# Kernel tuning notes

Hardware: AMD Instinct MI355X
Metric: run time of the kernel (lower is better)

The kernel has to match this reference:

```python
import jax, jax.numpy as jnp
import numpy as np
import math

D_MODEL = 256  # projected q/k dim
D_K_IN = 32    # raw key feature dim
D_V = 64       # value projection dim
KEEP_PROB = 0.8  # dropout p=0.2

def setup_inputs() -> dict:
    key = jax.random.key(0)
    ks = jax.random.split(key, 9)
    B, Lq, Lk = 4, 4096, 4096
    s = 0.02
    return {
        "q": jax.random.normal(ks[0], (B, Lq, D_MODEL), jnp.float32),
        "k": jax.random.normal(ks[1], (B, Lk, D_K_IN), jnp.float32),
        "v": jax.random.normal(ks[2], (B, Lk, D_MODEL), jnp.float32),
        "Wq": jax.random.normal(ks[3], (D_MODEL, D_MODEL), jnp.float32) * s,
        "bq": jnp.zeros((D_MODEL,), jnp.float32),
        "Wk": jax.random.normal(ks[4], (D_K_IN, D_MODEL), jnp.float32) * s,
        "bk": jnp.zeros((D_MODEL,), jnp.float32),
        "Wv": jax.random.normal(ks[5], (D_MODEL, D_V), jnp.float32) * s,
        "bv": jnp.zeros((D_V,), jnp.float32),
    }

def reference(q, k, v, Wq, bq, Wk, bk, Wv, bv):
    # Linear projections
    qp = q @ Wq + bq                       # [B, Lq, 256]
    kp = k @ Wk + bk                       # [B, Lk, 256]
    vp = v @ Wv + bv                       # [B, Lk, 64]
    scale = 1.0 / math.sqrt(qp.shape[-1])
    scores = jnp.einsum("bqd,bkd->bqk", qp, kp) * scale  # [B, Lq, Lk]
    attn = jax.nn.softmax(scores, axis=-1)
    # dropout p=0.2 (training mode), deterministic key
    mask = jax.random.bernoulli(jax.random.key(42), KEEP_PROB, attn.shape)
    attn = jnp.where(mask, attn / KEEP_PROB, 0.0)
    return jnp.einsum("bqk,bkd->bqd", attn, vp)  # [B, Lq, 64]
```

## Files before the change

### kernel.cpp

```cpp
#include <hip/hip_runtime.h>


typedef short s16x8 __attribute__((ext_vector_type(8)));
typedef float f32x4 __attribute__((ext_vector_type(4)));

#define L    4096
#define DM   256
#define DV   64
#define MTOT 16384

__device__ __forceinline__ short f2bf(float f) {
  unsigned u = __builtin_bit_cast(unsigned, f);
  u += 0x7FFFu + ((u >> 16) & 1u);
  return (short)(u >> 16);
}

__device__ __forceinline__ unsigned rotl32c(unsigned x, int r) {
  return (x << r) | (x >> (32 - r));
}

__device__ __forceinline__ unsigned tf_keep(unsigned ctr) {
  unsigned x0 = 0u;
  unsigned x1 = ctr + 42u;
#define TFR(r) { x0 += x1; x1 = rotl32c(x1, r); x1 ^= x0; }
  TFR(13) TFR(15) TFR(26) TFR(6)
  x0 += 42u;          x1 += 0x1BD11BF1u;
  TFR(17) TFR(29) TFR(16) TFR(24)
  x0 += 0x1BD11BF0u;  x1 += 2u;
  TFR(13) TFR(15) TFR(26) TFR(6)
         x1 += 45u;
  TFR(17) TFR(29) TFR(16) TFR(24)
  x0 += 42u;          x1 += 0x1BD11BF4u;
  TFR(13) TFR(15) TFR(26) TFR(6)
  x0 += 0x1BD11BF0u;  x1 += 5u;
#undef TFR
  return ((x0 ^ x1) < 3435974144u) ? 1u : 0u;
}

template <int K, int N, bool TRANS_OUT>
__global__ __launch_bounds__(256) void proj_kernel(
    const float* __restrict__ A, const float* __restrict__ W,
    const float* __restrict__ bias, short* __restrict__ out) {
  const int lane = threadIdx.x & 63;
  const int wv   = threadIdx.x >> 6;
  const int l15 = lane & 15, l4 = lane >> 4;
  const int rowbase = blockIdx.x * 64 + wv * 16;
  constexpr int NT = N / 16;
  constexpr int KC = K / 32;
  f32x4 acc[NT];
#pragma unroll
  for (int i = 0; i < NT; ++i) acc[i] = (f32x4){0.f, 0.f, 0.f, 0.f};
  const int arow = rowbase + l15;
  for (int kc = 0; kc < KC; ++kc) {
    const f32x4* ap = (const f32x4*)(A + (size_t)arow * K + kc * 32 + l4 * 8);
    f32x4 a0 = ap[0], a1 = ap[1];
    s16x8 af;
#pragma unroll
    for (int j = 0; j < 4; ++j) { af[j] = f2bf(a0[j]); af[4 + j] = f2bf(a1[j]); }
#pragma unroll
    for (int nt = 0; nt < NT; ++nt) {
      const float* wp = W + (size_t)(kc * 32 + l4 * 8) * N + nt * 16 + l15;
      s16x8 bf;
#pragma unroll
      for (int j = 0; j < 8; ++j) bf[j] = f2bf(wp[(size_t)j * N]);
      acc[nt] = __builtin_amdgcn_mfma_f32_16x16x32_bf16(af, bf, acc[nt], 0, 0, 0);
    }
  }
#pragma unroll
  for (int nt = 0; nt < NT; ++nt) {
    const int gcol = nt * 16 + l15;
    const float bv = bias[gcol];
#pragma unroll
    for (int j = 0; j < 4; ++j) {
      const int grow = rowbase + l4 * 4 + j;
      const float vv = acc[nt][j] + bv;
      if (TRANS_OUT) {
        const int b = grow >> 12, key = grow & 4095;
        out[(size_t)(b * 64 + gcol) * L + key] = f2bf(vv);
      } else {
        out[(size_t)grow * N + gcol] = f2bf(vv);
      }
    }
  }
}

__global__ __launch_bounds__(256) void attn_kernel(
    const short* __restrict__ qp, const short* __restrict__ kp,
    const short* __restrict__ vpT, float* __restrict__ out) {
  __shared__ __align__(16) short kbuf[64 * 256];
  __shared__ __align__(16) short vbuf[64 * 64];
  __shared__ __align__(16) short pbuf[4][16 * 64];
  const int tid = threadIdx.x;
  const int lane = tid & 63, wv = tid >> 6;
  const int l15 = lane & 15, l4 = lane >> 4;
  const int qt = blockIdx.x, b = blockIdx.y;
  const int qrow0 = b * L + qt * 64 + wv * 16;

  s16x8 qf[8];
#pragma unroll
  for (int kc = 0; kc < 8; ++kc)
    qf[kc] = *(const s16x8*)(qp + (size_t)(qrow0 + l15) * DM + kc * 32 + l4 * 8);

  f32x4 accO[4];
#pragma unroll
  for (int i = 0; i < 4; ++i) accO[i] = (f32x4){0.f, 0.f, 0.f, 0.f};
  float zpart[4] = {0.f, 0.f, 0.f, 0.f};

  const unsigned qglob = (unsigned)qrow0;
  constexpr float CEXP = 0.09016844005556021f;

  for (int kb = 0; kb < 64; ++kb) {
    __syncthreads();
    {
      const short* src = kp + (size_t)(b * L + kb * 64) * DM;
#pragma unroll
      for (int it = 0; it < 8; ++it) {
        const int c = it * 256 + tid;
        const int row = c >> 5, off = (c & 31) * 8;
        const int e = (row * 256 + off) ^ ((row & 7) << 3);
        *(s16x8*)(kbuf + e) = *(const s16x8*)(src + (size_t)row * DM + off);
      }
      const short* vsrc = vpT + (size_t)b * 64 * L + kb * 64;
#pragma unroll
      for (int it = 0; it < 2; ++it) {
        const int c = it * 256 + tid;
        const int row = c >> 3, off = (c & 7) * 8;
        const int e = (row * 64 + off) ^ ((row & 7) << 3);
        *(s16x8*)(vbuf + e) = *(const s16x8*)(vsrc + (size_t)row * L + off);
      }
    }
    __syncthreads();

    f32x4 sf[4];
#pragma unroll
    for (int kt = 0; kt < 4; ++kt) sf[kt] = (f32x4){0.f, 0.f, 0.f, 0.f};
#pragma unroll
    for (int kc = 0; kc < 8; ++kc) {
#pragma unroll
      for (int kt = 0; kt < 4; ++kt) {
        const int row = kt * 16 + l15;
        const int e = (row * 256 + kc * 32 + l4 * 8) ^ ((row & 7) << 3);
        const s16x8 kf = *(const s16x8*)(kbuf + e);
        sf[kt] = __builtin_amdgcn_mfma_f32_16x16x32_bf16(qf[kc], kf, sf[kt], 0, 0, 0);
      }
    }

    unsigned keep = 0;
#pragma unroll
    for (int kt = 0; kt < 4; ++kt) {
#pragma unroll
      for (int j = 0; j < 4; ++j) {
        const unsigned q = qglob + (unsigned)(l4 * 4 + j);
        const unsigned idx = (q << 12) + (unsigned)(kb * 64 + kt * 16 + l15);
        keep |= tf_keep(idx) << (kt * 4 + j);
      }
    }

#pragma unroll
    for (int kt = 0; kt < 4; ++kt) {
#pragma unroll
      for (int j = 0; j < 4; ++j) {
        const float e = exp2f(sf[kt][j] * CEXP);
        zpart[j] += e;
        const float pd = ((keep >> (kt * 4 + j)) & 1u) ? e : 0.0f;
        const int row = l4 * 4 + j, col = kt * 16 + l15;
        const int pe = (row * 64 + col) ^ ((row & 7) << 3);
        pbuf[wv][pe] = f2bf(pd);
      }
    }
    __syncthreads();

#pragma unroll
    for (int ks = 0; ks < 2; ++ks) {
      const int pe = (l15 * 64 + ks * 32 + l4 * 8) ^ ((l15 & 7) << 3);
      const s16x8 pa = *(const s16x8*)(&pbuf[wv][0] + pe);
#pragma unroll
      for (int nt = 0; nt < 4; ++nt) {
        const int vrow = nt * 16 + l15;
        const int ve = (vrow * 64 + ks * 32 + l4 * 8) ^ ((vrow & 7) << 3);
        const s16x8 vb = *(const s16x8*)(vbuf + ve);
        accO[nt] = __builtin_amdgcn_mfma_f32_16x16x32_bf16(pa, vb, accO[nt], 0, 0, 0);
      }
    }
  }

#pragma unroll
  for (int j = 0; j < 4; ++j) {
    float z = zpart[j];
    z += __shfl_xor(z, 1);
    z += __shfl_xor(z, 2);
    z += __shfl_xor(z, 4);
    z += __shfl_xor(z, 8);
    const float inv = 1.0f / (0.8f * z);
    const int grow = qrow0 + l4 * 4 + j;
#pragma unroll
    for (int nt = 0; nt < 4; ++nt)
      out[(size_t)grow * DV + nt * 16 + l15] = accO[nt][j] * inv;
  }
}

extern "C" void kernel_launch(void* const* d_in, const int* in_sizes, int n_in,
                              void* d_out, int out_size, void* d_ws, size_t ws_size,
                              hipStream_t stream) {
  const float* q  = (const float*)d_in[0];
  const float* k  = (const float*)d_in[1];
  const float* v  = (const float*)d_in[2];
  const float* Wq = (const float*)d_in[3];
  const float* bq = (const float*)d_in[4];
  const float* Wk = (const float*)d_in[5];
  const float* bk = (const float*)d_in[6];
  const float* Wv = (const float*)d_in[7];
  const float* bv = (const float*)d_in[8];
  float* out = (float*)d_out;

  short* qp  = (short*)d_ws;
  short* kpb = qp + (size_t)MTOT * DM;
  short* vpT = kpb + (size_t)MTOT * DM;

  proj_kernel<256, 256, false><<<MTOT / 64, 256, 0, stream>>>(q, Wq, bq, qp);
  proj_kernel<32, 256, false><<<MTOT / 64, 256, 0, stream>>>(k, Wk, bk, kpb);
  proj_kernel<256, 64, true><<<MTOT / 64, 256, 0, stream>>>(v, Wv, bv, vpT);
  attn_kernel<<<dim3(64, 4), 256, 0, stream>>>(qp, kpb, vpT, out);
}
```

Measured before the change: 384.8 us.

## Split attention over key dimension and pre-transpose bf16 projection weights

The attention kernel is split four ways along the key axis (grid z). Each split writes unnormalized partial outputs and partial softmax denominators, and a new combine kernel sums them and normalizes. This lifts the grid from 256 blocks to 1024 so the GPU is better filled, and the key tile shrinks to 32 rows to cut LDS use and raise occupancy. A prep kernel converts the weights to transposed bf16 once per call, so the projection kernels can do vector loads instead of strided scalar loads with per-element conversion. The cost is extra partial-result traffic to and from global memory plus two more kernel launches.

```diff
diff --git a/kernel.cpp b/kernel.cpp
--- a/kernel.cpp
+++ b/kernel.cpp
@@ -8,6 +8,8 @@
 #define DM   256
 #define DV   64
 #define MTOT 16384
+#define KSPLIT 4
+#define KBLK 32
 
 __device__ __forceinline__ short f2bf(float f) {
   unsigned u = __builtin_bit_cast(unsigned, f);
@@ -37,9 +39,28 @@
   return ((x0 ^ x1) < 3435974144u) ? 1u : 0u;
 }
 
+__global__ __launch_bounds__(256) void prep_kernel(
+    const float* __restrict__ Wq, const float* __restrict__ Wk,
+    const float* __restrict__ Wv, short* __restrict__ wqT,
+    short* __restrict__ wkT, short* __restrict__ wvT) {
+  const int idx = blockIdx.x * 256 + threadIdx.x;
+  if (idx < 65536) {
+    const int n = idx >> 8, k = idx & 255;
+    wqT[idx] = f2bf(Wq[k * 256 + n]);
+  }
+  if (idx < 8192) {
+    const int n = idx >> 5, k = idx & 31;
+    wkT[idx] = f2bf(Wk[k * 256 + n]);
+  }
+  if (idx < 16384) {
+    const int n = idx >> 8, k = idx & 255;
+    wvT[idx] = f2bf(Wv[k * 64 + n]);
+  }
+}
+
 template <int K, int N, bool TRANS_OUT>
 __global__ __launch_bounds__(256) void proj_kernel(
-    const float* __restrict__ A, const float* __restrict__ W,
+    const float* __restrict__ A, const short* __restrict__ WT,
     const float* __restrict__ bias, short* __restrict__ out) {
   const int lane = threadIdx.x & 63;
   const int wv   = threadIdx.x >> 6;
@@ -51,6 +72,7 @@
 #pragma unroll
   for (int i = 0; i < NT; ++i) acc[i] = (f32x4){0.f, 0.f, 0.f, 0.f};
   const int arow = rowbase + l15;
+#pragma unroll
   for (int kc = 0; kc < KC; ++kc) {
     const f32x4* ap = (const f32x4*)(A + (size_t)arow * K + kc * 32 + l4 * 8);
     f32x4 a0 = ap[0], a1 = ap[1];
@@ -59,10 +81,7 @@
     for (int j = 0; j < 4; ++j) { af[j] = f2bf(a0[j]); af[4 + j] = f2bf(a1[j]); }
 #pragma unroll
     for (int nt = 0; nt < NT; ++nt) {
-      const float* wp = W + (size_t)(kc * 32 + l4 * 8) * N + nt * 16 + l15;
-      s16x8 bf;
-#pragma unroll
-      for (int j = 0; j < 8; ++j) bf[j] = f2bf(wp[(size_t)j * N]);
+      const s16x8 bf = *(const s16x8*)(WT + (size_t)(nt * 16 + l15) * K + kc * 32 + l4 * 8);
       acc[nt] = __builtin_amdgcn_mfma_f32_16x16x32_bf16(af, bf, acc[nt], 0, 0, 0);
     }
   }
@@ -84,16 +103,17 @@
   }
 }
 
-__global__ __launch_bounds__(256) void attn_kernel(
+__global__ __launch_bounds__(256, 4) void attn_kernel(
     const short* __restrict__ qp, const short* __restrict__ kp,
-    const short* __restrict__ vpT, float* __restrict__ out) {
-  __shared__ __align__(16) short kbuf[64 * 256];
-  __shared__ __align__(16) short vbuf[64 * 64];
-  __shared__ __align__(16) short pbuf[4][16 * 64];
+    const short* __restrict__ vpT, float* __restrict__ partO,
+    float* __restrict__ partZ) {
+  __shared__ __align__(16) short kbuf[KBLK * 256];
+  __shared__ __align__(16) short vbuf[64 * KBLK];
+  __shared__ __align__(16) short pbuf[4][16 * KBLK];
   const int tid = threadIdx.x;
   const int lane = tid & 63, wv = tid >> 6;
   const int l15 = lane & 15, l4 = lane >> 4;
-  const int qt = blockIdx.x, b = blockIdx.y;
+  const int qt = blockIdx.x, b = blockIdx.y, z = blockIdx.z;
   const int qrow0 = b * L + qt * 64 + wv * 16;
 
   s16x8 qf[8];
@@ -108,36 +128,34 @@
 
   const unsigned qglob = (unsigned)qrow0;
   constexpr float CEXP = 0.09016844005556021f;
-
-  for (int kb = 0; kb < 64; ++kb) {
+  const int kb0 = z * (L / KSPLIT / KBLK);
+
+  for (int i = 0; i < L / KSPLIT / KBLK; ++i) {
+    const int kbase = (kb0 + i) * KBLK;
     __syncthreads();
     {
-      const short* src = kp + (size_t)(b * L + kb * 64) * DM;
-#pragma unroll
-      for (int it = 0; it < 8; ++it) {
+      const short* src = kp + (size_t)(b * L + kbase) * DM;
+#pragma unroll
+      for (int it = 0; it < 4; ++it) {
         const int c = it * 256 + tid;
         const int row = c >> 5, off = (c & 31) * 8;
         const int e = (row * 256 + off) ^ ((row & 7) << 3);
         *(s16x8*)(kbuf + e) = *(const s16x8*)(src + (size_t)row * DM + off);
       }
-      const short* vsrc = vpT + (size_t)b * 64 * L + kb * 64;
-#pragma unroll
-      for (int it = 0; it < 2; ++it) {
-        const int c = it * 256 + tid;
-        const int row = c >> 3, off = (c & 7) * 8;
-        const int e = (row * 64 + off) ^ ((row & 7) << 3);
-        *(s16x8*)(vbuf + e) = *(const s16x8*)(vsrc + (size_t)row * L + off);
-      }
+      const short* vsrc = vpT + (size_t)b * 64 * L + kbase;
+      const int row = tid >> 2, off = (tid & 3) * 8;
+      const int e = (row * KBLK + off) ^ ((row & 3) << 3);
+      *(s16x8*)(vbuf + e) = *(const s16x8*)(vsrc + (size_t)row * L + off);
     }
     __syncthreads();
 
-    f32x4 sf[4];
-#pragma unroll
-    for (int kt = 0; kt < 4; ++kt) sf[kt] = (f32x4){0.f, 0.f, 0.f, 0.f};
+    f32x4 sf[2];
+#pragma unroll
+    for (int kt = 0; kt < 2; ++kt) sf[kt] = (f32x4){0.f, 0.f, 0.f, 0.f};
 #pragma unroll
     for (int kc = 0; kc < 8; ++kc) {
 #pragma unroll
-      for (int kt = 0; kt < 4; ++kt) {
+      for (int kt = 0; kt < 2; ++kt) {
         const int row = kt * 16 + l15;
         const int e = (row * 256 + kc * 32 + l4 * 8) ^ ((row & 7) << 3);
         const s16x8 kf = *(const s16x8*)(kbuf + e);
@@ -147,37 +165,36 @@
 
     unsigned keep = 0;
 #pragma unroll
-    for (int kt = 0; kt < 4; ++kt) {
+    for (int kt = 0; kt < 2; ++kt) {
 #pragma unroll
       for (int j = 0; j < 4; ++j) {
         const unsigned q = qglob + (unsigned)(l4 * 4 + j);
-        const unsigned idx = (q << 12) + (unsigned)(kb * 64 + kt * 16 + l15);
+        const unsigned idx = (q << 12) + (unsigned)(kbase + kt * 16 + l15);
         keep |= tf_keep(idx) << (kt * 4 + j);
       }
     }
 
 #pragma unroll
-    for (int kt = 0; kt < 4; ++kt) {
+    for (int kt = 0; kt < 2; ++kt) {
 #pragma unroll
       for (int j = 0; j < 4; ++j) {
         const float e = exp2f(sf[kt][j] * CEXP);
         zpart[j] += e;
         const float pd = ((keep >> (kt * 4 + j)) & 1u) ? e : 0.0f;
         const int row = l4 * 4 + j, col = kt * 16 + l15;
-        const int pe = (row * 64 + col) ^ ((row & 7) << 3);
+        const int pe = (row * KBLK + col) ^ ((row & 3) << 3);
         pbuf[wv][pe] = f2bf(pd);
       }
     }
     __syncthreads();
 
-#pragma unroll
-    for (int ks = 0; ks < 2; ++ks) {
-      const int pe = (l15 * 64 + ks * 32 + l4 * 8) ^ ((l15 & 7) << 3);
+    {
+      const int pe = (l15 * KBLK + l4 * 8) ^ ((l15 & 3) << 3);
       const s16x8 pa = *(const s16x8*)(&pbuf[wv][0] + pe);
 #pragma unroll
       for (int nt = 0; nt < 4; ++nt) {
         const int vrow = nt * 16 + l15;
-        const int ve = (vrow * 64 + ks * 32 + l4 * 8) ^ ((vrow & 7) << 3);
+        const int ve = (vrow * KBLK + l4 * 8) ^ ((vrow & 3) << 3);
         const s16x8 vb = *(const s16x8*)(vbuf + ve);
         accO[nt] = __builtin_amdgcn_mfma_f32_16x16x32_bf16(pa, vb, accO[nt], 0, 0, 0);
       }
@@ -186,17 +203,34 @@
 
 #pragma unroll
   for (int j = 0; j < 4; ++j) {
-    float z = zpart[j];
-    z += __shfl_xor(z, 1);
-    z += __shfl_xor(z, 2);
-    z += __shfl_xor(z, 4);
-    z += __shfl_xor(z, 8);
-    const float inv = 1.0f / (0.8f * z);
+    float zf = zpart[j];
+    zf += __shfl_xor(zf, 1);
+    zf += __shfl_xor(zf, 2);
+    zf += __shfl_xor(zf, 4);
+    zf += __shfl_xor(zf, 8);
     const int grow = qrow0 + l4 * 4 + j;
+    if (l15 == 0) partZ[(size_t)z * MTOT + grow] = zf;
 #pragma unroll
     for (int nt = 0; nt < 4; ++nt)
-      out[(size_t)grow * DV + nt * 16 + l15] = accO[nt][j] * inv;
-  }
+      partO[((size_t)z * MTOT + grow) * DV + nt * 16 + l15] = accO[nt][j];
+  }
+}
+
+__global__ __launch_bounds__(256) void combine_kernel(
+    const float* __restrict__ partO, const float* __restrict__ partZ,
+    float* __restrict__ out) {
+  const int i = blockIdx.x * 256 + threadIdx.x;
+  const int row = i >> 4;
+  f32x4 acc = (f32x4){0.f, 0.f, 0.f, 0.f};
+  float zf = 0.f;
+#pragma unroll
+  for (int zz = 0; zz < KSPLIT; ++zz) {
+    acc += *(const f32x4*)(partO + (size_t)zz * MTOT * DV + (size_t)i * 4);
+    zf += partZ[(size_t)zz * MTOT + row];
+  }
+  const float inv = 1.0f / (0.8f * zf);
+  f32x4 r = acc * inv;
+  *(f32x4*)(out + (size_t)i * 4) = r;
 }
 
 extern "C" void kernel_launch(void* const* d_in, const int* in_sizes, int n_in,
@@ -216,9 +250,16 @@
   short* qp  = (short*)d_ws;
   short* kpb = qp + (size_t)MTOT * DM;
   short* vpT = kpb + (size_t)MTOT * DM;
-
-  proj_kernel<256, 256, false><<<MTOT / 64, 256, 0, stream>>>(q, Wq, bq, qp);
-  proj_kernel<32, 256, false><<<MTOT / 64, 256, 0, stream>>>(k, Wk, bk, kpb);
-  proj_kernel<256, 64, true><<<MTOT / 64, 256, 0, stream>>>(v, Wv, bv, vpT);
-  attn_kernel<<<dim3(64, 4), 256, 0, stream>>>(qp, kpb, vpT, out);
-}
+  float* partO = (float*)(vpT + (size_t)4 * 64 * L);
+  float* partZ = partO + (size_t)KSPLIT * MTOT * DV;
+  short* wqT = (short*)(partZ + (size_t)KSPLIT * MTOT);
+  short* wkT = wqT + 256 * 256;
+  short* wvT = wkT + 32 * 256;
+
+  prep_kernel<<<352, 256, 0, stream>>>(Wq, Wk, Wv, wqT, wkT, wvT);
+  proj_kernel<256, 256, false><<<MTOT / 64, 256, 0, stream>>>(q, wqT, bq, qp);
+  proj_kernel<32, 256, false><<<MTOT / 64, 256, 0, stream>>>(k, wkT, bk, kpb);
+  proj_kernel<256, 64, true><<<MTOT / 64, 256, 0, stream>>>(v, wvT, bv, vpT);
+  attn_kernel<<<dim3(64, 4, KSPLIT), 256, 0, stream>>>(qp, kpb, vpT, partO, partZ);
+  combine_kernel<<<MTOT * DV / 1024, 256, 0, stream>>>(partO, partZ, out);
+}
```

Result: faster. 364.1 us (-5.4%).
